# Performance work log

Measured on AMD Instinct MI355X. Metric: run time of the kernel, lower is better.

## Reference

```python
import jax, jax.numpy as jnp
import numpy as np

N_NODES = 100000
N_EDGES = 1600000
N_GRAPHS = 64
IN_DIM, HID_DIM, OUT_DIM = 128, 256, 256


def setup_inputs() -> dict:
    key = jax.random.key(0)
    ks = jax.random.split(key, 7)
    x = jax.random.normal(ks[0], (N_NODES, IN_DIM), dtype=jnp.float32)
    edge_index = jax.random.randint(ks[1], (2, N_EDGES), 0, N_NODES, dtype=jnp.int32)
    batch = jnp.sort(jax.random.randint(ks[2], (N_NODES,), 0, N_GRAPHS, dtype=jnp.int32))
    # Glorot-style init for GCN linear weights, zero bias (as in PyG defaults)
    W1 = jax.random.normal(ks[3], (IN_DIM, HID_DIM), dtype=jnp.float32) / np.sqrt(IN_DIM)
    b1 = jnp.zeros((HID_DIM,), dtype=jnp.float32)
    W2 = jax.random.normal(ks[4], (HID_DIM, OUT_DIM), dtype=jnp.float32) / np.sqrt(HID_DIM)
    b2 = jnp.zeros((OUT_DIM,), dtype=jnp.float32)
    return {"x": x, "edge_index": edge_index, "batch": batch,
            "W1": W1, "b1": b1, "W2": W2, "b2": b2}


def reference(x, edge_index, batch, W1, b1, W2, b2):
    N = x.shape[0]
    # --- GCN normalization with self-loops (computed once, edge structure fixed) ---
    loops = jnp.arange(N, dtype=edge_index.dtype)
    row = jnp.concatenate([edge_index[0], loops])  # source nodes  [E+N]
    col = jnp.concatenate([edge_index[1], loops])  # target nodes  [E+N]
    deg = jax.ops.segment_sum(jnp.ones_like(col, dtype=x.dtype), col, num_segments=N)
    dinv = jax.lax.rsqrt(jnp.maximum(deg, 1.0))    # deg >= 1 due to self-loops
    norm = dinv[row] * dinv[col]                   # [E+N]

    def gcn_conv(h, W, b):
        h = h @ W                                  # linear transform first (PyG order)
        msg = h[row] * norm[:, None]               # gather + normalize  [E+N, D]
        agg = jax.ops.segment_sum(msg, col, num_segments=N)  # scatter-add
        return agg + b

    h = jax.nn.relu(gcn_conv(x, W1, b1))
    h = jax.nn.relu(gcn_conv(h, W2, b2))

    # --- global mean pool over graph ids ---
    s = jax.ops.segment_sum(h, batch, num_segments=N_GRAPHS)           # [G, D]
    cnt = jax.ops.segment_sum(jnp.ones((N, 1), h.dtype), batch, num_segments=N_GRAPHS)
    return s / jnp.maximum(cnt, 1.0)
```

## Files before the change

kernel.cpp:

```cpp
#include <hip/hip_runtime.h>

typedef __attribute__((ext_vector_type(8))) short short8;
typedef __attribute__((ext_vector_type(4))) float float4v;

#define CAP 64
#define NPB 128
#define NCHUNK 8
#define BINCAP 384

__device__ __forceinline__ ushort f2bf(float f) {
    uint u = __float_as_uint(f);
    u += 0x7fffu + ((u >> 16) & 1u);
    return (ushort)(u >> 16);
}
__device__ __forceinline__ float bf2f(ushort h) {
    return __uint_as_float((uint)h << 16);
}
__device__ __forceinline__ void acc8(float* acc, uint4 v) {
    acc[0] += __uint_as_float(v.x << 16);
    acc[1] += __uint_as_float(v.x & 0xffff0000u);
    acc[2] += __uint_as_float(v.y << 16);
    acc[3] += __uint_as_float(v.y & 0xffff0000u);
    acc[4] += __uint_as_float(v.z << 16);
    acc[5] += __uint_as_float(v.z & 0xffff0000u);
    acc[6] += __uint_as_float(v.w << 16);
    acc[7] += __uint_as_float(v.w & 0xffff0000u);
}
__device__ __forceinline__ int clampi(int v, int n) {
    return (int)min((uint)v, (uint)(n - 1));
}

__global__ void zero_all_k(int* __restrict__ idg, float* __restrict__ out,
                           int* __restrict__ binCnt, int n, int nout, int nbc) {
    int i = blockIdx.x * 256 + threadIdx.x;
    if (i < n) idg[i] = 0;
    if (i < nout) out[i] = 0.f;
    if (i < nbc) binCnt[i] = 0;
}

__global__ void fillbin1_k(const int* __restrict__ row, const int* __restrict__ col,
                           int* __restrict__ idg, int* __restrict__ eidx,
                           int* __restrict__ binCnt, int2* __restrict__ binBuf,
                           int E, int nbins) {
    int e = blockIdx.x * 256 + threadIdx.x;
    int chunk = blockIdx.x & (NCHUNK - 1);
    if (e < E) {
        int c = col[e], r = row[e];
        int b = c >> 7;
        int cell = chunk * nbins + b;
        int p = atomicAdd(&binCnt[cell], 1);
        if (p < BINCAP) {
            binBuf[(size_t)cell * BINCAP + p] = make_int2(r, c);
        } else {
            int q = atomicAdd(&idg[c], 1);
            if (q < CAP) eidx[(size_t)c * CAP + q] = r;
        }
    }
}

__global__ __launch_bounds__(512) void fillbin2_k(const int* __restrict__ binCnt,
                                                  const int2* __restrict__ binBuf,
                                                  int* __restrict__ idg,
                                                  int* __restrict__ eidx, int nbins) {
    int bin = blockIdx.x;
    int wv = threadIdx.x >> 6, lane = threadIdx.x & 63;
    int cell = wv * nbins + bin;
    int n = min(binCnt[cell], BINCAP);
    const int2* bp = binBuf + (size_t)cell * BINCAP;
    for (int j = lane; j < n; j += 64) {
        int2 pr = bp[j];
        int c = pr.y;
        int p = atomicAdd(&idg[c], 1);
        if (p < CAP) eidx[(size_t)c * CAP + p] = pr.x;
    }
}

__global__ void prep_k(const float* __restrict__ W1, ushort* __restrict__ W1p,
                       const float* __restrict__ W2, ushort* __restrict__ W2p,
                       const float* __restrict__ x, const int* __restrict__ idg,
                       ushort* __restrict__ xb, int n4) {
    int idx = blockIdx.x * 256 + threadIdx.x;
    if (idx < 32768) {
        int j = idx & 7, lane = (idx >> 3) & 63;
        int s = (idx >> 9) % 4, nt = (idx >> 9) / 4;
        int k = 32 * s + (lane >> 4) * 8 + j;
        int c = nt * 16 + (lane & 15);
        W1p[idx] = f2bf(W1[k * 256 + c]);
    } else if (idx < 32768 + 65536) {
        int q = idx - 32768;
        int j = q & 7, lane = (q >> 3) & 63;
        int s = (q >> 9) % 8, nt = (q >> 9) / 8;
        int k = 32 * s + (lane >> 4) * 8 + j;
        int c = nt * 16 + (lane & 15);
        W2p[q] = f2bf(W2[k * 256 + c]);
    } else {
        int i = idx - (32768 + 65536);
        if (i < n4) {
            int node = i >> 5;
            float di = rsqrtf((float)(idg[node] + 1));
            float4 v = ((const float4*)x)[i];
            ushort4 o;
            o.x = f2bf(v.x * di); o.y = f2bf(v.y * di);
            o.z = f2bf(v.z * di); o.w = f2bf(v.w * di);
            ((ushort4*)xb)[i] = o;
        }
    }
}

__global__ __launch_bounds__(256) void agg128_k(const ushort* __restrict__ g,
                                                ushort* __restrict__ out,
                                                const int* __restrict__ idg,
                                                const int* __restrict__ eidx, int n) {
    int w = threadIdx.x >> 6, lane = threadIdx.x & 63;
    int q = lane >> 4, sub = lane & 15;
    int i = blockIdx.x * 16 + w * 4 + q;
    if (i >= n) return;
    const ushort* gp = g + (size_t)sub * 8;
    float acc[8] = {};
    {
        uint4 v = *(const uint4*)(gp + (size_t)i * 128);
        acc8(acc, v);
    }
    int deg = idg[i];
    int cnt = min(deg, CAP);
    const int* ep = eidx + (size_t)i * CAP;
    int j = 0;
    for (; j + 8 <= cnt; j += 8) {
        int s0 = clampi(ep[j], n),     s1 = clampi(ep[j + 1], n);
        int s2 = clampi(ep[j + 2], n), s3 = clampi(ep[j + 3], n);
        int s4 = clampi(ep[j + 4], n), s5 = clampi(ep[j + 5], n);
        int s6 = clampi(ep[j + 6], n), s7 = clampi(ep[j + 7], n);
        uint4 v0 = *(const uint4*)(gp + (size_t)s0 * 128);
        uint4 v1 = *(const uint4*)(gp + (size_t)s1 * 128);
        uint4 v2 = *(const uint4*)(gp + (size_t)s2 * 128);
        uint4 v3 = *(const uint4*)(gp + (size_t)s3 * 128);
        uint4 v4 = *(const uint4*)(gp + (size_t)s4 * 128);
        uint4 v5 = *(const uint4*)(gp + (size_t)s5 * 128);
        uint4 v6 = *(const uint4*)(gp + (size_t)s6 * 128);
        uint4 v7 = *(const uint4*)(gp + (size_t)s7 * 128);
        acc8(acc, v0); acc8(acc, v1); acc8(acc, v2); acc8(acc, v3);
        acc8(acc, v4); acc8(acc, v5); acc8(acc, v6); acc8(acc, v7);
    }
    if (j + 4 <= cnt) {
        int s0 = clampi(ep[j], n),     s1 = clampi(ep[j + 1], n);
        int s2 = clampi(ep[j + 2], n), s3 = clampi(ep[j + 3], n);
        uint4 v0 = *(const uint4*)(gp + (size_t)s0 * 128);
        uint4 v1 = *(const uint4*)(gp + (size_t)s1 * 128);
        uint4 v2 = *(const uint4*)(gp + (size_t)s2 * 128);
        uint4 v3 = *(const uint4*)(gp + (size_t)s3 * 128);
        acc8(acc, v0); acc8(acc, v1); acc8(acc, v2); acc8(acc, v3);
        j += 4;
    }
    if (j + 2 <= cnt) {
        int s0 = clampi(ep[j], n), s1 = clampi(ep[j + 1], n);
        uint4 v0 = *(const uint4*)(gp + (size_t)s0 * 128);
        uint4 v1 = *(const uint4*)(gp + (size_t)s1 * 128);
        acc8(acc, v0); acc8(acc, v1);
        j += 2;
    }
    if (j < cnt) {
        int s0 = clampi(ep[j], n);
        uint4 v0 = *(const uint4*)(gp + (size_t)s0 * 128);
        acc8(acc, v0);
    }
    float di = rsqrtf((float)(deg + 1));
    uint4 o;
    o.x = (uint)f2bf(acc[0] * di) | ((uint)f2bf(acc[1] * di) << 16);
    o.y = (uint)f2bf(acc[2] * di) | ((uint)f2bf(acc[3] * di) << 16);
    o.z = (uint)f2bf(acc[4] * di) | ((uint)f2bf(acc[5] * di) << 16);
    o.w = (uint)f2bf(acc[6] * di) | ((uint)f2bf(acc[7] * di) << 16);
    *(uint4*)(out + (size_t)i * 128 + sub * 8) = o;
}

__global__ __launch_bounds__(256) void agg256_k(const ushort* __restrict__ g,
                                                ushort* __restrict__ out,
                                                const int* __restrict__ idg,
                                                const int* __restrict__ eidx, int n) {
    int w = threadIdx.x >> 6, lane = threadIdx.x & 63;
    int half = lane >> 5, sub = lane & 31;
    int i = blockIdx.x * 8 + w * 2 + half;
    if (i >= n) return;
    const ushort* gp = g + (size_t)sub * 8;
    float acc[8] = {};
    {
        uint4 v = *(const uint4*)(gp + (size_t)i * 256);
        acc8(acc, v);
    }
    int deg = idg[i];
    int cnt = min(deg, CAP);
    const int* ep = eidx + (size_t)i * CAP;
    int j = 0;
    for (; j + 8 <= cnt; j += 8) {
        int s0 = clampi(ep[j], n),     s1 = clampi(ep[j + 1], n);
        int s2 = clampi(ep[j + 2], n), s3 = clampi(ep[j + 3], n);
        int s4 = clampi(ep[j + 4], n), s5 = clampi(ep[j + 5], n);
        int s6 = clampi(ep[j + 6], n), s7 = clampi(ep[j + 7], n);
        uint4 v0 = *(const uint4*)(gp + (size_t)s0 * 256);
        uint4 v1 = *(const uint4*)(gp + (size_t)s1 * 256);
        uint4 v2 = *(const uint4*)(gp + (size_t)s2 * 256);
        uint4 v3 = *(const uint4*)(gp + (size_t)s3 * 256);
        uint4 v4 = *(const uint4*)(gp + (size_t)s4 * 256);
        uint4 v5 = *(const uint4*)(gp + (size_t)s5 * 256);
        uint4 v6 = *(const uint4*)(gp + (size_t)s6 * 256);
        uint4 v7 = *(const uint4*)(gp + (size_t)s7 * 256);
        acc8(acc, v0); acc8(acc, v1); acc8(acc, v2); acc8(acc, v3);
        acc8(acc, v4); acc8(acc, v5); acc8(acc, v6); acc8(acc, v7);
    }
    if (j + 4 <= cnt) {
        int s0 = clampi(ep[j], n),     s1 = clampi(ep[j + 1], n);
        int s2 = clampi(ep[j + 2], n), s3 = clampi(ep[j + 3], n);
        uint4 v0 = *(const uint4*)(gp + (size_t)s0 * 256);
        uint4 v1 = *(const uint4*)(gp + (size_t)s1 * 256);
        uint4 v2 = *(const uint4*)(gp + (size_t)s2 * 256);
        uint4 v3 = *(const uint4*)(gp + (size_t)s3 * 256);
        acc8(acc, v0); acc8(acc, v1); acc8(acc, v2); acc8(acc, v3);
        j += 4;
    }
    if (j + 2 <= cnt) {
        int s0 = clampi(ep[j], n), s1 = clampi(ep[j + 1], n);
        uint4 v0 = *(const uint4*)(gp + (size_t)s0 * 256);
        uint4 v1 = *(const uint4*)(gp + (size_t)s1 * 256);
        acc8(acc, v0); acc8(acc, v1);
        j += 2;
    }
    if (j < cnt) {
        int s0 = clampi(ep[j], n);
        uint4 v0 = *(const uint4*)(gp + (size_t)s0 * 256);
        acc8(acc, v0);
    }
    float di = rsqrtf((float)(deg + 1));
    uint4 o;
    o.x = (uint)f2bf(acc[0] * di) | ((uint)f2bf(acc[1] * di) << 16);
    o.y = (uint)f2bf(acc[2] * di) | ((uint)f2bf(acc[3] * di) << 16);
    o.z = (uint)f2bf(acc[4] * di) | ((uint)f2bf(acc[5] * di) << 16);
    o.w = (uint)f2bf(acc[6] * di) | ((uint)f2bf(acc[7] * di) << 16);
    *(uint4*)(out + (size_t)i * 256 + sub * 8) = o;
}

template <int K, bool SCALE>
__global__ __launch_bounds__(256) void gemm_ldsw_k(const ushort* __restrict__ A,
                                                   const ushort* __restrict__ Wp,
                                                   const float* __restrict__ bias,
                                                   const int* __restrict__ idg,
                                                   ushort* __restrict__ C, int M) {
    constexpr int S = K / 32;
    constexpr int STAGE_US = 4 * S * 64 * 8;
    __shared__ ushort ldsW[STAGE_US];
    int tid = threadIdx.x, wv = tid >> 6, lane = tid & 63;
    int quad = lane >> 4, l15 = lane & 15;
    int rowBase = blockIdx.x * 64 + wv * 16;
    int arow = rowBase + l15; if (arow > M - 1) arow = M - 1;
    const ushort* abase = A + (size_t)arow * K + quad * 8;
    short8 af[S];
#pragma unroll
    for (int s = 0; s < S; ++s) af[s] = *(const short8*)(abase + 32 * s);

    float diRow[4];
    if (SCALE) {
#pragma unroll
        for (int r = 0; r < 4; ++r) {
            int rr = min(rowBase + quad * 4 + r, M - 1);
            diRow[r] = rsqrtf((float)(idg[rr] + 1));
        }
    }

#pragma unroll
    for (int st = 0; st < 4; ++st) {
        __syncthreads();
        {
            const uint4* src = (const uint4*)(Wp + (size_t)st * STAGE_US);
            uint4* dst = (uint4*)ldsW;
#pragma unroll
            for (int it = 0; it < STAGE_US / 8 / 256; ++it)
                dst[it * 256 + tid] = src[it * 256 + tid];
        }
        __syncthreads();
        float4v acc[4];
#pragma unroll
        for (int nt = 0; nt < 4; ++nt) {
            float4v a = {0.f, 0.f, 0.f, 0.f};
#pragma unroll
            for (int s = 0; s < S; ++s) {
                short8 bf = *(const short8*)&ldsW[((nt * S + s) * 64 + lane) * 8];
                a = __builtin_amdgcn_mfma_f32_16x16x32_bf16(af[s], bf, a, 0, 0, 0);
            }
            acc[nt] = a;
        }
#pragma unroll
        for (int nt = 0; nt < 4; ++nt) {
            int col = (st * 4 + nt) * 16 + l15;
            float b = bias[col];
#pragma unroll
            for (int r = 0; r < 4; ++r) {
                int row = rowBase + quad * 4 + r;
                if (row < M) {
                    float v = fmaxf(acc[nt][r] + b, 0.f);
                    if (SCALE) v *= diRow[r];
                    C[(size_t)row * 256 + col] = f2bf(v);
                }
            }
        }
    }
}

__global__ void pool_k(const ushort* __restrict__ h, const int* __restrict__ batch,
                       float* __restrict__ outsum, int n) {
    int d = threadIdx.x;
    int n0 = blockIdx.x * 128;
    int n1 = min(n0 + 128, n);
    int gcur = -1;
    float sum = 0.f;
    for (int nn = n0; nn < n1; ++nn) {
        int g = batch[nn] & 63;
        float v = bf2f(h[(size_t)nn * 256 + d]);
        if (g != gcur) {
            if (gcur >= 0) atomicAdd(&outsum[gcur * 256 + d], sum);
            gcur = g;
            sum = v;
        } else {
            sum += v;
        }
    }
    if (gcur >= 0) atomicAdd(&outsum[gcur * 256 + d], sum);
}

__global__ void final_k(float* __restrict__ out, const int* __restrict__ batch, int n) {
    __shared__ float cntS;
    int g = blockIdx.x, d = threadIdx.x;
    if (d == 0) {
        int lo = 0, hi = n;
        while (lo < hi) { int mid = (lo + hi) >> 1; if (batch[mid] < g) lo = mid + 1; else hi = mid; }
        int s = lo;
        lo = 0; hi = n;
        int g1 = g + 1;
        while (lo < hi) { int mid = (lo + hi) >> 1; if (batch[mid] < g1) lo = mid + 1; else hi = mid; }
        cntS = (float)(lo - s);
    }
    __syncthreads();
    out[g * 256 + d] /= fmaxf(cntS, 1.0f);
}

extern "C" void kernel_launch(void* const* d_in, const int* in_sizes, int n_in,
                              void* d_out, int out_size, void* d_ws, size_t ws_size,
                              hipStream_t stream) {
    const float* x  = (const float*)d_in[0];
    const int*   ei = (const int*)d_in[1];
    const int*   batch = (const int*)d_in[2];
    const float* W1 = (const float*)d_in[3];
    const float* b1 = (const float*)d_in[4];
    const float* W2 = (const float*)d_in[5];
    const float* b2 = (const float*)d_in[6];
    float* out = (float*)d_out;

    const int N  = in_sizes[2];
    const int E  = in_sizes[1] / 2;
    const int* row = ei;
    const int* col = ei + E;

    char* p = (char*)d_ws;
    auto alloc = [&](size_t bytes) {
        char* q = p;
        p += (bytes + 255) & ~(size_t)255;
        return q;
    };
    int*    idg    = (int*)alloc((size_t)N * 4);
    int*    eidx   = (int*)alloc((size_t)N * CAP * 4);
    ushort* W1p    = (ushort*)alloc(16 * 4 * 64 * 8 * 2);
    ushort* W2p    = (ushort*)alloc(16 * 8 * 64 * 8 * 2);
    ushort* xb     = (ushort*)alloc((size_t)N * 128 * 2);
    ushort* aggX   = (ushort*)alloc((size_t)N * 128 * 2);
    ushort* g1     = (ushort*)alloc((size_t)N * 256 * 2);
    ushort* aggH   = (ushort*)alloc((size_t)N * 256 * 2);
    ushort* h2     = (ushort*)alloc((size_t)N * 256 * 2);

    const int nbins = (N + NPB - 1) >> 7;
    const int nbc   = NCHUNK * nbins;
    int*    binCnt = (int*)alloc((size_t)nbc * 4);
    int2*   binBuf = (int2*)h2;

    const int nb  = (N + 255) / 256;
    const int ebl = (E + 255) / 256;

    zero_all_k<<<nb, 256, 0, stream>>>(idg, out, binCnt, N, out_size, nbc);

    fillbin1_k<<<ebl, 256, 0, stream>>>(row, col, idg, eidx, binCnt, binBuf, E, nbins);
    fillbin2_k<<<nbins, 512, 0, stream>>>(binCnt, binBuf, idg, eidx, nbins);

    const int n4 = N * 32;
    prep_k<<<(98304 + n4 + 255) / 256, 256, 0, stream>>>(W1, W1p, W2, W2p, x, idg, xb, n4);

    agg128_k<<<(N + 15) / 16, 256, 0, stream>>>(xb, aggX, idg, eidx, N);
    const int gb = (N + 63) / 64;
    gemm_ldsw_k<128, true><<<gb, 256, 0, stream>>>(aggX, W1p, b1, idg, g1, N);

    agg256_k<<<(N + 7) / 8, 256, 0, stream>>>(g1, aggH, idg, eidx, N);
    gemm_ldsw_k<256, false><<<gb, 256, 0, stream>>>(aggH, W2p, b2, nullptr, h2, N);

    pool_k<<<(N + 127) / 128, 256, 0, stream>>>(h2, batch, out, N);
    final_k<<<64, 256, 0, stream>>>(out, batch, N);
}
```

Baseline: 540.4 us.

## Replace two-pass binned adjacency fill with direct atomic fill and nontemporal accesses

Drops the chunked bin staging (fillbin1/fillbin2) in favour of a single kernel that atomically increments per-node in-degree and writes source indices straight into the CAP-wide adjacency table, using nontemporal stores. The aggregation kernels now read edge indices with nontemporal loads and write their bf16 outputs with nontemporal stores, aiming to cut cache pollution and one kernel launch plus the bin-buffer traffic. The trade-off is scattered atomics and stores across the whole idg/eidx arrays, which the binning was meant to localise.

```diff
diff --git a/kernel.cpp b/kernel.cpp
--- a/kernel.cpp
+++ b/kernel.cpp
@@ -2,11 +2,9 @@
 
 typedef __attribute__((ext_vector_type(8))) short short8;
 typedef __attribute__((ext_vector_type(4))) float float4v;
+typedef __attribute__((ext_vector_type(4))) uint uint4v;
 
 #define CAP 64
-#define NPB 128
-#define NCHUNK 8
-#define BINCAP 384
 
 __device__ __forceinline__ ushort f2bf(float f) {
     uint u = __float_as_uint(f);
@@ -31,47 +29,20 @@
 }
 
 __global__ void zero_all_k(int* __restrict__ idg, float* __restrict__ out,
-                           int* __restrict__ binCnt, int n, int nout, int nbc) {
+                           int n, int nout) {
     int i = blockIdx.x * 256 + threadIdx.x;
     if (i < n) idg[i] = 0;
     if (i < nout) out[i] = 0.f;
-    if (i < nbc) binCnt[i] = 0;
-}
-
-__global__ void fillbin1_k(const int* __restrict__ row, const int* __restrict__ col,
-                           int* __restrict__ idg, int* __restrict__ eidx,
-                           int* __restrict__ binCnt, int2* __restrict__ binBuf,
-                           int E, int nbins) {
+}
+
+__global__ void fill_k(const int* __restrict__ row, const int* __restrict__ col,
+                       int* __restrict__ idg, int* __restrict__ eidx, int E) {
     int e = blockIdx.x * 256 + threadIdx.x;
-    int chunk = blockIdx.x & (NCHUNK - 1);
     if (e < E) {
-        int c = col[e], r = row[e];
-        int b = c >> 7;
-        int cell = chunk * nbins + b;
-        int p = atomicAdd(&binCnt[cell], 1);
-        if (p < BINCAP) {
-            binBuf[(size_t)cell * BINCAP + p] = make_int2(r, c);
-        } else {
-            int q = atomicAdd(&idg[c], 1);
-            if (q < CAP) eidx[(size_t)c * CAP + q] = r;
-        }
-    }
-}
-
-__global__ __launch_bounds__(512) void fillbin2_k(const int* __restrict__ binCnt,
-                                                  const int2* __restrict__ binBuf,
-                                                  int* __restrict__ idg,
-                                                  int* __restrict__ eidx, int nbins) {
-    int bin = blockIdx.x;
-    int wv = threadIdx.x >> 6, lane = threadIdx.x & 63;
-    int cell = wv * nbins + bin;
-    int n = min(binCnt[cell], BINCAP);
-    const int2* bp = binBuf + (size_t)cell * BINCAP;
-    for (int j = lane; j < n; j += 64) {
-        int2 pr = bp[j];
-        int c = pr.y;
+        int c = col[e];
+        int r = row[e];
         int p = atomicAdd(&idg[c], 1);
-        if (p < CAP) eidx[(size_t)c * CAP + p] = pr.x;
+        if (p < CAP) __builtin_nontemporal_store(r, eidx + (size_t)c * CAP + p);
     }
 }
 
@@ -126,10 +97,14 @@
     const int* ep = eidx + (size_t)i * CAP;
     int j = 0;
     for (; j + 8 <= cnt; j += 8) {
-        int s0 = clampi(ep[j], n),     s1 = clampi(ep[j + 1], n);
-        int s2 = clampi(ep[j + 2], n), s3 = clampi(ep[j + 3], n);
-        int s4 = clampi(ep[j + 4], n), s5 = clampi(ep[j + 5], n);
-        int s6 = clampi(ep[j + 6], n), s7 = clampi(ep[j + 7], n);
+        int s0 = clampi(__builtin_nontemporal_load(ep + j), n);
+        int s1 = clampi(__builtin_nontemporal_load(ep + j + 1), n);
+        int s2 = clampi(__builtin_nontemporal_load(ep + j + 2), n);
+        int s3 = clampi(__builtin_nontemporal_load(ep + j + 3), n);
+        int s4 = clampi(__builtin_nontemporal_load(ep + j + 4), n);
+        int s5 = clampi(__builtin_nontemporal_load(ep + j + 5), n);
+        int s6 = clampi(__builtin_nontemporal_load(ep + j + 6), n);
+        int s7 = clampi(__builtin_nontemporal_load(ep + j + 7), n);
         uint4 v0 = *(const uint4*)(gp + (size_t)s0 * 128);
         uint4 v1 = *(const uint4*)(gp + (size_t)s1 * 128);
         uint4 v2 = *(const uint4*)(gp + (size_t)s2 * 128);
@@ -142,8 +117,10 @@
         acc8(acc, v4); acc8(acc, v5); acc8(acc, v6); acc8(acc, v7);
     }
     if (j + 4 <= cnt) {
-        int s0 = clampi(ep[j], n),     s1 = clampi(ep[j + 1], n);
-        int s2 = clampi(ep[j + 2], n), s3 = clampi(ep[j + 3], n);
+        int s0 = clampi(__builtin_nontemporal_load(ep + j), n);
+        int s1 = clampi(__builtin_nontemporal_load(ep + j + 1), n);
+        int s2 = clampi(__builtin_nontemporal_load(ep + j + 2), n);
+        int s3 = clampi(__builtin_nontemporal_load(ep + j + 3), n);
         uint4 v0 = *(const uint4*)(gp + (size_t)s0 * 128);
         uint4 v1 = *(const uint4*)(gp + (size_t)s1 * 128);
         uint4 v2 = *(const uint4*)(gp + (size_t)s2 * 128);
@@ -152,24 +129,25 @@
         j += 4;
     }
     if (j + 2 <= cnt) {
-        int s0 = clampi(ep[j], n), s1 = clampi(ep[j + 1], n);
+        int s0 = clampi(__builtin_nontemporal_load(ep + j), n);
+        int s1 = clampi(__builtin_nontemporal_load(ep + j + 1), n);
         uint4 v0 = *(const uint4*)(gp + (size_t)s0 * 128);
         uint4 v1 = *(const uint4*)(gp + (size_t)s1 * 128);
         acc8(acc, v0); acc8(acc, v1);
         j += 2;
     }
     if (j < cnt) {
-        int s0 = clampi(ep[j], n);
+        int s0 = clampi(__builtin_nontemporal_load(ep + j), n);
         uint4 v0 = *(const uint4*)(gp + (size_t)s0 * 128);
         acc8(acc, v0);
     }
     float di = rsqrtf((float)(deg + 1));
-    uint4 o;
+    uint4v o;
     o.x = (uint)f2bf(acc[0] * di) | ((uint)f2bf(acc[1] * di) << 16);
     o.y = (uint)f2bf(acc[2] * di) | ((uint)f2bf(acc[3] * di) << 16);
     o.z = (uint)f2bf(acc[4] * di) | ((uint)f2bf(acc[5] * di) << 16);
     o.w = (uint)f2bf(acc[6] * di) | ((uint)f2bf(acc[7] * di) << 16);
-    *(uint4*)(out + (size_t)i * 128 + sub * 8) = o;
+    __builtin_nontemporal_store(o, (uint4v*)(out + (size_t)i * 128 + sub * 8));
 }
 
 __global__ __launch_bounds__(256) void agg256_k(const ushort* __restrict__ g,
@@ -191,10 +169,14 @@
     const int* ep = eidx + (size_t)i * CAP;
     int j = 0;
     for (; j + 8 <= cnt; j += 8) {
-        int s0 = clampi(ep[j], n),     s1 = clampi(ep[j + 1], n);
-        int s2 = clampi(ep[j + 2], n), s3 = clampi(ep[j + 3], n);
-        int s4 = clampi(ep[j + 4], n), s5 = clampi(ep[j + 5], n);
-        int s6 = clampi(ep[j + 6], n), s7 = clampi(ep[j + 7], n);
+        int s0 = clampi(__builtin_nontemporal_load(ep + j), n);
+        int s1 = clampi(__builtin_nontemporal_load(ep + j + 1), n);
+        int s2 = clampi(__builtin_nontemporal_load(ep + j + 2), n);
+        int s3 = clampi(__builtin_nontemporal_load(ep + j + 3), n);
+        int s4 = clampi(__builtin_nontemporal_load(ep + j + 4), n);
+        int s5 = clampi(__builtin_nontemporal_load(ep + j + 5), n);
+        int s6 = clampi(__builtin_nontemporal_load(ep + j + 6), n);
+        int s7 = clampi(__builtin_nontemporal_load(ep + j + 7), n);
         uint4 v0 = *(const uint4*)(gp + (size_t)s0 * 256);
         uint4 v1 = *(const uint4*)(gp + (size_t)s1 * 256);
         uint4 v2 = *(const uint4*)(gp + (size_t)s2 * 256);
@@ -207,8 +189,10 @@
         acc8(acc, v4); acc8(acc, v5); acc8(acc, v6); acc8(acc, v7);
     }
     if (j + 4 <= cnt) {
-        int s0 = clampi(ep[j], n),     s1 = clampi(ep[j + 1], n);
-        int s2 = clampi(ep[j + 2], n), s3 = clampi(ep[j + 3], n);
+        int s0 = clampi(__builtin_nontemporal_load(ep + j), n);
+        int s1 = clampi(__builtin_nontemporal_load(ep + j + 1), n);
+        int s2 = clampi(__builtin_nontemporal_load(ep + j + 2), n);
+        int s3 = clampi(__builtin_nontemporal_load(ep + j + 3), n);
         uint4 v0 = *(const uint4*)(gp + (size_t)s0 * 256);
         uint4 v1 = *(const uint4*)(gp + (size_t)s1 * 256);
         uint4 v2 = *(const uint4*)(gp + (size_t)s2 * 256);
@@ -217,24 +201,25 @@
         j += 4;
     }
     if (j + 2 <= cnt) {
-        int s0 = clampi(ep[j], n), s1 = clampi(ep[j + 1], n);
+        int s0 = clampi(__builtin_nontemporal_load(ep + j), n);
+        int s1 = clampi(__builtin_nontemporal_load(ep + j + 1), n);
         uint4 v0 = *(const uint4*)(gp + (size_t)s0 * 256);
         uint4 v1 = *(const uint4*)(gp + (size_t)s1 * 256);
         acc8(acc, v0); acc8(acc, v1);
         j += 2;
     }
     if (j < cnt) {
-        int s0 = clampi(ep[j], n);
+        int s0 = clampi(__builtin_nontemporal_load(ep + j), n);
         uint4 v0 = *(const uint4*)(gp + (size_t)s0 * 256);
         acc8(acc, v0);
     }
     float di = rsqrtf((float)(deg + 1));
-    uint4 o;
+    uint4v o;
     o.x = (uint)f2bf(acc[0] * di) | ((uint)f2bf(acc[1] * di) << 16);
     o.y = (uint)f2bf(acc[2] * di) | ((uint)f2bf(acc[3] * di) << 16);
     o.z = (uint)f2bf(acc[4] * di) | ((uint)f2bf(acc[5] * di) << 16);
     o.w = (uint)f2bf(acc[6] * di) | ((uint)f2bf(acc[7] * di) << 16);
-    *(uint4*)(out + (size_t)i * 256 + sub * 8) = o;
+    __builtin_nontemporal_store(o, (uint4v*)(out + (size_t)i * 256 + sub * 8));
 }
 
 template <int K, bool SCALE>
@@ -373,18 +358,12 @@
     ushort* aggH   = (ushort*)alloc((size_t)N * 256 * 2);
     ushort* h2     = (ushort*)alloc((size_t)N * 256 * 2);
 
-    const int nbins = (N + NPB - 1) >> 7;
-    const int nbc   = NCHUNK * nbins;
-    int*    binCnt = (int*)alloc((size_t)nbc * 4);
-    int2*   binBuf = (int2*)h2;
-
     const int nb  = (N + 255) / 256;
     const int ebl = (E + 255) / 256;
 
-    zero_all_k<<<nb, 256, 0, stream>>>(idg, out, binCnt, N, out_size, nbc);
-
-    fillbin1_k<<<ebl, 256, 0, stream>>>(row, col, idg, eidx, binCnt, binBuf, E, nbins);
-    fillbin2_k<<<nbins, 512, 0, stream>>>(binCnt, binBuf, idg, eidx, nbins);
+    zero_all_k<<<nb, 256, 0, stream>>>(idg, out, N, out_size);
+
+    fill_k<<<ebl, 256, 0, stream>>>(row, col, idg, eidx, E);
 
     const int n4 = N * 32;
     prep_k<<<(98304 + n4 + 255) / 256, 256, 0, stream>>>(W1, W1p, W2, W2p, x, idg, xb, n4);
```

Result: no change. 547.8 us (+1.4%).
